# Kernel tuning notes

Measured on AMD Instinct MI355X. Metric: run time of the kernel, lower is better.

## Reference

```python
import jax, jax.numpy as jnp
import numpy as np

B, T, E = 32, 2048, 128

def setup_inputs() -> dict:
    key = jax.random.key(0)
    ks = jax.random.split(key, 6)
    return {
        "x1": jax.random.normal(ks[0], (B, T, E), dtype=jnp.float32),
        "x2": jax.random.normal(ks[1], (B, T, E), dtype=jnp.float32),
        "W1": jax.random.normal(ks[2], (E, 1), dtype=jnp.float32) * 0.05,
        "b1": jnp.zeros((T, 1), dtype=jnp.float32),
        "U1": jax.random.normal(ks[3], (E, T), dtype=jnp.float32) * 0.05,
        "W2": jax.random.normal(ks[4], (E, 1), dtype=jnp.float32) * 0.05,
        "b2": jnp.zeros((T, 1), dtype=jnp.float32),
        "U2": jax.random.normal(ks[5], (E, T), dtype=jnp.float32) * 0.05,
    }


def reference(x1, x2, W1, b1, U1, W2, b2, U2):
    # S[b,i,j] = <x1[b,i], x2[b,j]>  -> (B, T, T)
    S = jnp.einsum('bie,bje->bij', x1, x2)
    inv_T = jnp.float32(1.0) / S.shape[1]
    # c1 = mean_j sum_i S[b,i,j] * x2[b,i,e]  -> (B, E)
    c1 = jnp.einsum('bij,bie->be', S, x2) * inv_T
    # c2 = mean_i sum_j S[b,i,j] * x1[b,j,e]  -> (B, E)
    c2 = jnp.einsum('bij,bje->be', S, x1) * inv_T
    # attention logits: (B, T)
    et1 = c1 @ U1 + jnp.squeeze(x1 @ W1 + b1, axis=-1)
    et2 = c2 @ U2 + jnp.squeeze(x2 @ W2 + b2, axis=-1)
    at1 = jax.nn.softmax(et1, axis=-1)
    at2 = jax.nn.softmax(et2, axis=-1)
    # attention-weighted sums: (B, E)
    o1 = jnp.einsum('bt,bte->be', at1, x1)
    o2 = jnp.einsum('bt,bte->be', at2, x2)
    # merge_mode == 'concat'
    return jnp.concatenate([o1, o2], axis=1)
```

## Files before the change

### kernel.cpp

```cpp
#include <hip/hip_runtime.h>


#define B_ 32
#define T_ 2048
#define E_ 128
#define EV (E_/4)
#define INV_T (1.0f/2048.0f)
#define RC 128
#define NG (T_/RC)

#define WS_PSX1 0
#define WS_PSX2 65536
#define WS_PM   131072
#define WS_ET1  8519680
#define WS_ET2  8585216
#define WS_C1   8650752
#define WS_C2   8683520

__device__ __forceinline__ float dot4(float4 a, float4 b) {
    return a.x*b.x + a.y*b.y + a.z*b.z + a.w*b.w;
}
__device__ __forceinline__ void fma4(float4& a, float s, const float4 v) {
    a.x += s*v.x; a.y += s*v.y; a.z += s*v.z; a.w += s*v.w;
}
__device__ __forceinline__ void add4(float4& a, const float4 v) {
    a.x += v.x; a.y += v.y; a.z += v.z; a.w += v.w;
}

__global__ __launch_bounds__(256)
void ka_gram(const float* __restrict__ x1, const float* __restrict__ x2,
             const float* __restrict__ W1, const float* __restrict__ b1,
             const float* __restrict__ W2, const float* __restrict__ b2,
             float* __restrict__ ws) {
    __shared__ float4 sb[2][64][32];
    __shared__ float4 sW[2][32];
    const int b = blockIdx.x, g = blockIdx.y, tid = threadIdx.x;
    if (tid < 64) sW[tid>>5][tid&31] = ((const float4*)((tid<32) ? W1 : W2))[tid&31];
    __syncthreads();

    const int q = tid & 15, rr = tid >> 4;
    const int ty = tid >> 4, tx = tid & 15;

    const float4* x1g = (const float4*)x1 + ((size_t)b*T_ + g*RC)*EV;
    const float4* x2g = (const float4*)x2 + ((size_t)b*T_ + g*RC)*EV;

    float4 acc[16];
    #pragma unroll
    for (int i = 0; i < 16; ++i) acc[i] = make_float4(0.f,0.f,0.f,0.f);
    float4 ps[4];
    #pragma unroll
    for (int i = 0; i < 4; ++i) ps[i] = make_float4(0.f,0.f,0.f,0.f);

    for (int s = 0; s < 2; ++s) {
        #pragma unroll
        for (int ten = 0; ten < 2; ++ten) {
            const float4* xg = ten ? x2g : x1g;
            float* etp = ws + (ten ? WS_ET2 : WS_ET1) + (size_t)b*T_;
            const float* bias = ten ? b2 : b1;
            #pragma unroll
            for (int i = 0; i < 4; ++i) {
                const int row = rr + i*16;
                const float4* p = xg + (size_t)(s*64 + row)*EV + 2*q;
                const float4 n0 = p[0], n1 = p[1];
                add4(ps[ten*2+0], n0); add4(ps[ten*2+1], n1);
                float d = dot4(n0, sW[ten][2*q]) + dot4(n1, sW[ten][2*q+1]);
                d += __shfl_xor(d, 1); d += __shfl_xor(d, 2);
                d += __shfl_xor(d, 4); d += __shfl_xor(d, 8);
                if (q == 0) {
                    const int t = g*RC + s*64 + row;
                    etp[t] = d + bias[t];
                }
                sb[ten][row][q]      = n0;
                sb[ten][row][16 + q] = n1;
            }
        }
        __syncthreads();
        #pragma unroll 8
        for (int t = 0; t < 64; ++t) {
            const float4 a0  = sb[1][t][ty];
            const float4 a1  = sb[1][t][16 + ty];
            const float4 bv0 = sb[0][t][tx];
            const float4 bv1 = sb[0][t][16 + tx];
            const float ae[8] = {a0.x,a0.y,a0.z,a0.w,a1.x,a1.y,a1.z,a1.w};
            #pragma unroll
            for (int i = 0; i < 8; ++i) {
                fma4(acc[2*i+0], ae[i], bv0);
                fma4(acc[2*i+1], ae[i], bv1);
            }
        }
        __syncthreads();
    }

    float4* pMW = (float4*)(ws + WS_PM) + (size_t)(b*NG + g)*4096;
    #pragma unroll
    for (int i = 0; i < 8; ++i) {
        pMW[(ty*8 + i)*32 + 2*tx + 0] = acc[2*i+0];
        pMW[(ty*8 + i)*32 + 2*tx + 1] = acc[2*i+1];
    }

    float4* spx = &sb[0][0][0];
    spx[tid] = ps[0]; spx[256 + tid] = ps[1];
    spx[512 + tid] = ps[2]; spx[768 + tid] = ps[3];
    __syncthreads();
    if (tid < 64) {
        const int pt = tid>>5, c4 = tid&31, qq = c4>>1, h = c4&1;
        float4 sum = {0,0,0,0};
        #pragma unroll
        for (int r = 0; r < 16; ++r) add4(sum, spx[pt*512 + h*256 + r*16 + qq]);
        ((float4*)(ws + (pt ? WS_PSX2 : WS_PSX1)))[(size_t)(b*NG + g)*32 + c4] = sum;
    }
}

__global__ __launch_bounds__(256)
void kb_c(float* __restrict__ ws) {
    __shared__ float4 ssx1v[32], ssx2v[32];
    __shared__ float4 c2p[8][32];
    const int b = blockIdx.x, gs = blockIdx.y, tid = threadIdx.x;
    float* ssx1 = (float*)ssx1v;
    float* ssx2 = (float*)ssx2v;
    if (tid < 128) {
        float s = 0.f;
        #pragma unroll
        for (int g = 0; g < NG; ++g) s += ws[WS_PSX2 + (size_t)(b*NG + g)*E_ + tid];
        ssx2[tid] = s;
    } else {
        float s = 0.f;
        #pragma unroll
        for (int g = 0; g < NG; ++g) s += ws[WS_PSX1 + (size_t)(b*NG + g)*E_ + (tid-128)];
        ssx1[tid-128] = s;
    }
    __syncthreads();
    const int hw = tid>>5, j = tid&31;
    const float4* pM4 = (const float4*)(ws + WS_PM) + (size_t)b*NG*4096;
    const float4 sxj = ssx2v[j];
    float4 c2a = {0,0,0,0};
    #pragma unroll
    for (int r = 0; r < 16; ++r) {
        const int e = hw*16 + r;
        const float s1 = ssx1[e];
        float ca = 0.f;
        #pragma unroll
        for (int g2 = 0; g2 < 2; ++g2) {
            float4 v = pM4[(size_t)(gs*2 + g2)*4096 + e*32 + j];
            ca += dot4(v, sxj);
            fma4(c2a, s1, v);
        }
        #pragma unroll
        for (int m = 1; m <= 16; m <<= 1) ca += __shfl_xor(ca, m);
        if (j == 0) ws[WS_C1 + (size_t)(b*8 + gs)*E_ + e] = ca * INV_T;
    }
    c2p[hw][j] = c2a;
    __syncthreads();
    if (tid < 128) {
        float s = 0.f;
        #pragma unroll
        for (int h = 0; h < 8; ++h) s += ((const float*)c2p)[h*128 + tid];
        ws[WS_C2 + (size_t)(b*8 + gs)*E_ + tid] = s * INV_T;
    }
}

__global__ __launch_bounds__(256)
void kc_etU(const float* __restrict__ U1, const float* __restrict__ U2,
            float* __restrict__ ws) {
    __shared__ float s_c[B_][E_];
    const int ch = blockIdx.x, sel = blockIdx.y, tid = threadIdx.x;
    const float4* c4g = (const float4*)(ws + (sel ? WS_C2 : WS_C1));
    float4* s_c4 = (float4*)&s_c[0][0];
    #pragma unroll
    for (int i = 0; i < 4; ++i) {
        const int idx = tid + 256*i;
        const int base = (idx & ~31)*8 + (idx & 31);
        float4 s = {0,0,0,0};
        #pragma unroll
        for (int gs = 0; gs < 8; ++gs) add4(s, c4g[base + gs*32]);
        s_c4[idx] = s;
    }
    __syncthreads();
    const float4* U4 = (const float4*)(sel ? U2 : U1);
    const int c4i = tid&31, bg = tid>>5;
    float4 acc[4];
    #pragma unroll
    for (int q = 0; q < 4; ++q) acc[q] = make_float4(0.f,0.f,0.f,0.f);
    #pragma unroll 4
    for (int e = 0; e < E_; ++e) {
        const float4 u = U4[(size_t)e*(T_/4) + ch*32 + c4i];
        fma4(acc[0], s_c[bg*4+0][e], u);
        fma4(acc[1], s_c[bg*4+1][e], u);
        fma4(acc[2], s_c[bg*4+2][e], u);
        fma4(acc[3], s_c[bg*4+3][e], u);
    }
    float4* et4 = (float4*)(ws + (sel ? WS_ET2 : WS_ET1));
    #pragma unroll
    for (int q = 0; q < 4; ++q) {
        const int bb = bg*4 + q;
        const size_t idx = (size_t)bb*(T_/4) + ch*32 + c4i;
        float4 v = et4[idx];
        add4(v, acc[q]);
        et4[idx] = v;
    }
}

__global__ __launch_bounds__(512)
void kd_softmax(float* __restrict__ ws, float* __restrict__ out) {
    __shared__ float red[512];
    const int b = blockIdx.x, sel = blockIdx.y, tid = threadIdx.x;
    float4* et4 = (float4*)(ws + (sel ? WS_ET2 : WS_ET1) + (size_t)b*T_);
    float4 v = et4[tid];
    if (tid < E_) out[b*2*E_ + sel*E_ + tid] = 0.f;
    float m = fmaxf(fmaxf(v.x, v.y), fmaxf(v.z, v.w));
    red[tid] = m; __syncthreads();
    for (int s = 256; s > 0; s >>= 1) {
        if (tid < s) red[tid] = fmaxf(red[tid], red[tid+s]);
        __syncthreads();
    }
    m = red[0]; __syncthreads();
    float4 e4;
    e4.x = __expf(v.x - m); e4.y = __expf(v.y - m);
    e4.z = __expf(v.z - m); e4.w = __expf(v.w - m);
    red[tid] = e4.x + e4.y + e4.z + e4.w;
    __syncthreads();
    for (int s = 256; s > 0; s >>= 1) {
        if (tid < s) red[tid] += red[tid+s];
        __syncthreads();
    }
    const float il = 1.f / red[0];
    e4.x *= il; e4.y *= il; e4.z *= il; e4.w *= il;
    et4[tid] = e4;
}

__global__ __launch_bounds__(256)
void ke_out(const float* __restrict__ x1, const float* __restrict__ x2,
            const float* __restrict__ ws, float* __restrict__ out) {
    __shared__ float4 s_r1[256], s_r2[256];
    __shared__ float s_p1[128], s_p2[128];
    const int b = blockIdx.x, g = blockIdx.y, tid = threadIdx.x;
    const float* pr1 = ws + WS_ET1 + (size_t)b*T_ + g*128;
    const float* pr2 = ws + WS_ET2 + (size_t)b*T_ + g*128;
    if (tid < 128) s_p1[tid] = pr1[tid];
    else           s_p2[tid - 128] = pr2[tid - 128];
    __syncthreads();
    const float4* p1 = (const float4*)x1 + ((size_t)b*T_ + g*128)*EV;
    const float4* p2 = (const float4*)x2 + ((size_t)b*T_ + g*128)*EV;
    const int rg = tid >> 5, q = tid & 31;
    float4 a1 = {0,0,0,0}, a2 = {0,0,0,0};
    #pragma unroll
    for (int i = 0; i < 16; ++i) {
        int r = i*8 + rg;
        fma4(a1, s_p1[r], p1[r*EV + q]);
        fma4(a2, s_p2[r], p2[r*EV + q]);
    }
    s_r1[tid] = a1; s_r2[tid] = a2;
    __syncthreads();
    for (int s = 128; s >= 32; s >>= 1) {
        if (tid < s) { add4(s_r1[tid], s_r1[tid+s]); add4(s_r2[tid], s_r2[tid+s]); }
        __syncthreads();
    }
    if (tid < 32) {
        float4 t1 = s_r1[tid], t2 = s_r2[tid];
        atomicAdd(&out[b*2*E_ + tid*4+0], t1.x);
        atomicAdd(&out[b*2*E_ + tid*4+1], t1.y);
        atomicAdd(&out[b*2*E_ + tid*4+2], t1.z);
        atomicAdd(&out[b*2*E_ + tid*4+3], t1.w);
        atomicAdd(&out[b*2*E_ + E_ + tid*4+0], t2.x);
        atomicAdd(&out[b*2*E_ + E_ + tid*4+1], t2.y);
        atomicAdd(&out[b*2*E_ + E_ + tid*4+2], t2.z);
        atomicAdd(&out[b*2*E_ + E_ + tid*4+3], t2.w);
    }
}

extern "C" void kernel_launch(void* const* d_in, const int* in_sizes, int n_in,
                              void* d_out, int out_size, void* d_ws, size_t ws_size,
                              hipStream_t stream) {
    const float* x1 = (const float*)d_in[0];
    const float* x2 = (const float*)d_in[1];
    const float* W1 = (const float*)d_in[2];
    const float* b1 = (const float*)d_in[3];
    const float* U1 = (const float*)d_in[4];
    const float* W2 = (const float*)d_in[5];
    const float* b2 = (const float*)d_in[6];
    const float* U2 = (const float*)d_in[7];
    float* ws  = (float*)d_ws;
    float* out = (float*)d_out;

    ka_gram<<<dim3(B_, NG), 256, 0, stream>>>(x1, x2, W1, b1, W2, b2, ws);
    kb_c<<<dim3(B_, 8), 256, 0, stream>>>(ws);
    kc_etU<<<dim3(16, 2), 256, 0, stream>>>(U1, U2, ws);
    kd_softmax<<<dim3(B_, 2), 512, 0, stream>>>(ws, out);
    ke_out<<<dim3(B_, 16), 256, 0, stream>>>(x1, x2, ws, out);
}
```

Before: 182.9 us.

## Compute per-chunk Gram matrix with split-bf16 MFMA instead of FP32 FMA

The per-chunk E×E outer-product accumulation (x2ᵀ·x1 over 128 rows) in ka_gram now runs on bf16 MFMA 16x16x32 instructions. Each fp32 value is split into high and low bf16 parts, and three MFMA passes (hi·hi, hi·lo, lo·hi) recover near-fp32 accuracy. The inputs are transposed into a swizzled LDS layout to avoid bank conflicts, and the load mapping is changed so the bias dot products are reduced with a 32-lane shuffle. The aim is to cut the scalar FMA cost of the Gram stage, at the price of extra packing work and a small loss of precision from dropping the lo·lo term.

```diff
diff --git a/kernel.cpp b/kernel.cpp
--- a/kernel.cpp
+++ b/kernel.cpp
@@ -17,6 +17,9 @@
 #define WS_C1   8650752
 #define WS_C2   8683520
 
+typedef __attribute__((ext_vector_type(8))) short short8;
+typedef __attribute__((ext_vector_type(4))) float f32x4;
+
 __device__ __forceinline__ float dot4(float4 a, float4 b) {
     return a.x*b.x + a.y*b.y + a.z*b.z + a.w*b.w;
 }
@@ -25,6 +28,37 @@
 }
 __device__ __forceinline__ void add4(float4& a, const float4 v) {
     a.x += v.x; a.y += v.y; a.z += v.z; a.w += v.w;
+}
+
+__device__ __forceinline__ unsigned swz(int e, unsigned tbyte) {
+    return tbyte ^ ((((unsigned)e & 3u) << 3) | ((((unsigned)e >> 2) & 3u) << 5));
+}
+
+__device__ __forceinline__ void pack_hilo(float f0, float f1, float f2, float f3,
+                                          unsigned long long& wh,
+                                          unsigned long long& wl) {
+    unsigned u0 = __float_as_uint(f0), u1 = __float_as_uint(f1);
+    unsigned u2 = __float_as_uint(f2), u3 = __float_as_uint(f3);
+    unsigned h0 = u0 & 0xFFFF0000u, h1 = u1 & 0xFFFF0000u;
+    unsigned h2 = u2 & 0xFFFF0000u, h3 = u3 & 0xFFFF0000u;
+    unsigned hw0 = h1 | (h0 >> 16);
+    unsigned hw1 = h3 | (h2 >> 16);
+    unsigned l0 = __float_as_uint(f0 - __uint_as_float(h0));
+    unsigned l1 = __float_as_uint(f1 - __uint_as_float(h1));
+    unsigned l2 = __float_as_uint(f2 - __uint_as_float(h2));
+    unsigned l3 = __float_as_uint(f3 - __uint_as_float(h3));
+    unsigned lw0 = (l1 & 0xFFFF0000u) | (l0 >> 16);
+    unsigned lw1 = (l3 & 0xFFFF0000u) | (l2 >> 16);
+    wh = ((unsigned long long)hw1 << 32) | hw0;
+    wl = ((unsigned long long)lw1 << 32) | lw0;
+}
+
+__device__ __forceinline__ short8 frag_ld(const char* buf, int row, int t0) {
+    unsigned a1 = (unsigned)row * 128u + swz(row, (unsigned)t0 * 2u);
+    union { unsigned long long u[2]; short8 v; } r;
+    r.u[0] = *(const unsigned long long*)(buf + a1);
+    r.u[1] = *(const unsigned long long*)(buf + (a1 ^ 32u));
+    return r.v;
 }
 
 __global__ __launch_bounds__(256)
@@ -32,82 +66,116 @@
              const float* __restrict__ W1, const float* __restrict__ b1,
              const float* __restrict__ W2, const float* __restrict__ b2,
              float* __restrict__ ws) {
-    __shared__ float4 sb[2][64][32];
+    __shared__ unsigned short ldsq[4][128][64];
     __shared__ float4 sW[2][32];
     const int b = blockIdx.x, g = blockIdx.y, tid = threadIdx.x;
     if (tid < 64) sW[tid>>5][tid&31] = ((const float4*)((tid<32) ? W1 : W2))[tid&31];
     __syncthreads();
 
-    const int q = tid & 15, rr = tid >> 4;
-    const int ty = tid >> 4, tx = tid & 15;
+    const int eq = tid & 31, tp = tid >> 5;
+    const int lane = tid & 63, w = tid >> 6;
 
     const float4* x1g = (const float4*)x1 + ((size_t)b*T_ + g*RC)*EV;
     const float4* x2g = (const float4*)x2 + ((size_t)b*T_ + g*RC)*EV;
 
-    float4 acc[16];
-    #pragma unroll
-    for (int i = 0; i < 16; ++i) acc[i] = make_float4(0.f,0.f,0.f,0.f);
-    float4 ps[4];
-    #pragma unroll
-    for (int i = 0; i < 4; ++i) ps[i] = make_float4(0.f,0.f,0.f,0.f);
+    float4 psA1 = {0,0,0,0}, psA2 = {0,0,0,0};
+    f32x4 acc[2][8];
+    #pragma unroll
+    for (int i = 0; i < 2; ++i)
+        #pragma unroll
+        for (int j = 0; j < 8; ++j) acc[i][j] = (f32x4){0.f,0.f,0.f,0.f};
+
+    char* Lb = (char*)&ldsq[0][0][0];
+    const char* Apass[3] = { Lb + 2*16384, Lb + 2*16384, Lb + 3*16384 };
+    const char* Bpass[3] = { Lb + 0,       Lb + 1*16384, Lb + 0       };
 
     for (int s = 0; s < 2; ++s) {
         #pragma unroll
-        for (int ten = 0; ten < 2; ++ten) {
-            const float4* xg = ten ? x2g : x1g;
-            float* etp = ws + (ten ? WS_ET2 : WS_ET1) + (size_t)b*T_;
-            const float* bias = ten ? b2 : b1;
+        for (int u = 0; u < 4; ++u) {
+            const int ten = u >> 1;
+            const int tq  = tp + (u & 1)*8;
+            const int tl  = tq*4;
+            const int tr  = s*64 + tl;
+            const float4* src = (ten ? x2g : x1g) + (size_t)tr*EV + eq;
+            const float4 v0 = src[0], v1 = src[EV], v2 = src[2*EV], v3 = src[3*EV];
+            float4& ps = ten ? psA2 : psA1;
+            add4(ps, v0); add4(ps, v1); add4(ps, v2); add4(ps, v3);
+            const float4 wv = sW[ten][eq];
+            float d0 = dot4(v0,wv), d1 = dot4(v1,wv), d2 = dot4(v2,wv), d3 = dot4(v3,wv);
             #pragma unroll
-            for (int i = 0; i < 4; ++i) {
-                const int row = rr + i*16;
-                const float4* p = xg + (size_t)(s*64 + row)*EV + 2*q;
-                const float4 n0 = p[0], n1 = p[1];
-                add4(ps[ten*2+0], n0); add4(ps[ten*2+1], n1);
-                float d = dot4(n0, sW[ten][2*q]) + dot4(n1, sW[ten][2*q+1]);
-                d += __shfl_xor(d, 1); d += __shfl_xor(d, 2);
-                d += __shfl_xor(d, 4); d += __shfl_xor(d, 8);
-                if (q == 0) {
-                    const int t = g*RC + s*64 + row;
-                    etp[t] = d + bias[t];
+            for (int mm = 1; mm <= 16; mm <<= 1) {
+                d0 += __shfl_xor(d0, mm); d1 += __shfl_xor(d1, mm);
+                d2 += __shfl_xor(d2, mm); d3 += __shfl_xor(d3, mm);
+            }
+            if (eq == 0) {
+                const int tg = g*RC + tr;
+                const float4 bb = *(const float4*)((ten ? b2 : b1) + tg);
+                *(float4*)(ws + (ten ? WS_ET2 : WS_ET1) + (size_t)b*T_ + tg)
+                    = make_float4(d0+bb.x, d1+bb.y, d2+bb.z, d3+bb.w);
+            }
+            char* Hb = Lb + (ten ? 2 : 0)*16384;
+            char* Lo = Hb + 16384;
+            const unsigned tb = (unsigned)tl * 2u;
+            unsigned long long wh, wl;
+            {   const int e = eq*4 + 0; const unsigned off = (unsigned)e*128u + swz(e, tb);
+                pack_hilo(v0.x, v1.x, v2.x, v3.x, wh, wl);
+                *(unsigned long long*)(Hb + off) = wh;
+                *(unsigned long long*)(Lo + off) = wl; }
+            {   const int e = eq*4 + 1; const unsigned off = (unsigned)e*128u + swz(e, tb);
+                pack_hilo(v0.y, v1.y, v2.y, v3.y, wh, wl);
+                *(unsigned long long*)(Hb + off) = wh;
+                *(unsigned long long*)(Lo + off) = wl; }
+            {   const int e = eq*4 + 2; const unsigned off = (unsigned)e*128u + swz(e, tb);
+                pack_hilo(v0.z, v1.z, v2.z, v3.z, wh, wl);
+                *(unsigned long long*)(Hb + off) = wh;
+                *(unsigned long long*)(Lo + off) = wl; }
+            {   const int e = eq*4 + 3; const unsigned off = (unsigned)e*128u + swz(e, tb);
+                pack_hilo(v0.w, v1.w, v2.w, v3.w, wh, wl);
+                *(unsigned long long*)(Hb + off) = wh;
+                *(unsigned long long*)(Lo + off) = wl; }
+        }
+        __syncthreads();
+        #pragma unroll
+        for (int pass = 0; pass < 3; ++pass) {
+            #pragma unroll
+            for (int ks = 0; ks < 2; ++ks) {
+                const int t0 = ks*32 + ((lane>>4)<<2);
+                const short8 a0 = frag_ld(Apass[pass], w*32 + (lane&15), t0);
+                const short8 a1 = frag_ld(Apass[pass], w*32 + 16 + (lane&15), t0);
+                #pragma unroll
+                for (int ft = 0; ft < 8; ++ft) {
+                    const short8 bv = frag_ld(Bpass[pass], ft*16 + (lane&15), t0);
+                    acc[0][ft] = __builtin_amdgcn_mfma_f32_16x16x32_bf16(a0, bv, acc[0][ft], 0, 0, 0);
+                    acc[1][ft] = __builtin_amdgcn_mfma_f32_16x16x32_bf16(a1, bv, acc[1][ft], 0, 0, 0);
                 }
-                sb[ten][row][q]      = n0;
-                sb[ten][row][16 + q] = n1;
             }
         }
         __syncthreads();
-        #pragma unroll 8
-        for (int t = 0; t < 64; ++t) {
-            const float4 a0  = sb[1][t][ty];
-            const float4 a1  = sb[1][t][16 + ty];
-            const float4 bv0 = sb[0][t][tx];
-            const float4 bv1 = sb[0][t][16 + tx];
-            const float ae[8] = {a0.x,a0.y,a0.z,a0.w,a1.x,a1.y,a1.z,a1.w};
+    }
+
+    float* pM = ws + WS_PM + (size_t)(b*NG + g)*16384;
+    #pragma unroll
+    for (int et = 0; et < 2; ++et) {
+        #pragma unroll
+        for (int ft = 0; ft < 8; ++ft) {
             #pragma unroll
-            for (int i = 0; i < 8; ++i) {
-                fma4(acc[2*i+0], ae[i], bv0);
-                fma4(acc[2*i+1], ae[i], bv1);
+            for (int r = 0; r < 4; ++r) {
+                const int e = w*32 + et*16 + ((lane>>4)<<2) + r;
+                const int f = ft*16 + (lane&15);
+                pM[e*128 + f] = acc[et][ft][r];
             }
         }
-        __syncthreads();
-    }
-
-    float4* pMW = (float4*)(ws + WS_PM) + (size_t)(b*NG + g)*4096;
-    #pragma unroll
-    for (int i = 0; i < 8; ++i) {
-        pMW[(ty*8 + i)*32 + 2*tx + 0] = acc[2*i+0];
-        pMW[(ty*8 + i)*32 + 2*tx + 1] = acc[2*i+1];
-    }
-
-    float4* spx = &sb[0][0][0];
-    spx[tid] = ps[0]; spx[256 + tid] = ps[1];
-    spx[512 + tid] = ps[2]; spx[768 + tid] = ps[3];
+    }
+
+    float4* spx = (float4*)Lb;
+    spx[tid*2 + 0] = psA1; spx[tid*2 + 1] = psA2;
     __syncthreads();
     if (tid < 64) {
-        const int pt = tid>>5, c4 = tid&31, qq = c4>>1, h = c4&1;
+        const int ten = tid>>5, eqq = tid&31;
         float4 sum = {0,0,0,0};
         #pragma unroll
-        for (int r = 0; r < 16; ++r) add4(sum, spx[pt*512 + h*256 + r*16 + qq]);
-        ((float4*)(ws + (pt ? WS_PSX2 : WS_PSX1)))[(size_t)(b*NG + g)*32 + c4] = sum;
+        for (int t2 = 0; t2 < 8; ++t2) add4(sum, spx[(t2*32 + eqq)*2 + ten]);
+        ((float4*)(ws + (ten ? WS_PSX2 : WS_PSX1)))[(size_t)(b*NG + g)*32 + eqq] = sum;
     }
 }
 
```

Result: faster. 165.4 us (-9.6%).
